# Performance work log

Measured on AMD Instinct MI355X. Metric: run time of the kernel, lower is better.

The kernel has to match this reference:

```python
import jax, jax.numpy as jnp
import numpy as np

B, S, D, H, R = 16, 2048, 1024, 1024, 16


def setup_inputs() -> dict:
    key = jax.random.key(0)
    ks = jax.random.split(key, 6)
    inv = 1.0 / np.sqrt(D)
    return {
        "x": jax.random.normal(ks[0], (B, S, D), jnp.float32),
        "Wa": jax.random.uniform(ks[1], (H, D), jnp.float32, -inv, inv),
        "ba": jnp.zeros((H,), jnp.float32),
        "Wg": jax.random.uniform(ks[2], (R, D), jnp.float32, -inv, inv),
        "bg": jnp.zeros((R,), jnp.float32),
        "Wu": jax.random.uniform(ks[3], (H, D), jnp.float32, -inv, inv),
        "bu": jnp.zeros((H,), jnp.float32),
        "u": jax.random.normal(ks[4], (H, R), jnp.float32) * 0.02,
        "v": jax.random.normal(ks[5], (H, R), jnp.float32) * 0.02,
    }


def reference(x, Wa, ba, Wg, bg, Wu, bu, u, v):
    # Precompute all per-step projections in big GEMMs (same math as the
    # per-step Linear calls in the original loop).
    a = jax.nn.sigmoid(jnp.einsum('bsd,hd->bsh', x, Wa) + ba)   # [B,S,H]
    g = jnp.einsum('bsd,rd->bsr', x, Wg) + bg                    # [B,S,R]
    u_in = jnp.einsum('bsd,hd->bsh', x, Wu) + bu                 # [B,S,H]

    def step(state, ins):
        a_t, g_t, u_t = ins                      # [B,H], [B,R], [B,H]
        low_rank = (state @ v) * g_t             # [B,R]
        state = a_t * state + u_t + low_rank @ u.T
        return state, None

    init = jnp.zeros((x.shape[0], Wa.shape[0]), x.dtype)
    seq = (jnp.swapaxes(a, 0, 1), jnp.swapaxes(g, 0, 1), jnp.swapaxes(u_in, 0, 1))
    state, _ = jax.lax.scan(step, init, seq)
    return state  # [B, H]
```

## Files before the change

### kernel.cpp

```cpp
#include <hip/hip_runtime.h>
#include <hip/hip_bf16.h>
#include <stdint.h>

#define Bb 16
#define Ss 2048
#define Dd 1024
#define Hh 1024
#define Rr 16
#define Mm 32768

typedef __attribute__((ext_vector_type(4))) float f32x4;
typedef __attribute__((ext_vector_type(8))) short bf16x8;

__device__ __forceinline__ unsigned short f2bf(float f) {
    union { float f; uint32_t u; } c; c.f = f;
    uint32_t u = c.u + 0x7fffu + ((c.u >> 16) & 1u);
    return (unsigned short)(u >> 16);
}
__device__ __forceinline__ float bfbits2f(uint32_t bits) {
    union { uint32_t u; float f; } c; c.u = bits << 16; return c.f;
}

__device__ __forceinline__ void gld16(const void* gsrc, void* ldst) {
    __builtin_amdgcn_global_load_lds(
        (const __attribute__((address_space(1))) unsigned int*)gsrc,
        (__attribute__((address_space(3))) unsigned int*)ldst, 16, 0, 0);
}

__device__ __forceinline__ void softbar() {
    __asm volatile("" ::: "memory");
    __builtin_amdgcn_s_waitcnt(0xC07F);
    __builtin_amdgcn_s_barrier();
    __asm volatile("" ::: "memory");
}

__global__ __launch_bounds__(256) void k_convert(
    const float* __restrict__ x, const float* __restrict__ Wa,
    const float* __restrict__ Wu,
    unsigned short* __restrict__ xb, unsigned short* __restrict__ Wab,
    unsigned short* __restrict__ Wub)
{
    long e = ((long)blockIdx.x * 256 + threadIdx.x) * 4;
    const long nx = (long)Mm * Dd;
    const long nw = (long)Hh * Dd;
    const float* src; unsigned short* dst; long o;
    if (e < nx)            { src = x;  dst = xb;  o = e; }
    else if (e < nx + nw)  { src = Wa; dst = Wab; o = e - nx; }
    else                   { src = Wu; dst = Wub; o = e - nx - nw; }
    float4 f = *(const float4*)(src + o);
    ushort4 r;
    r.x = f2bf(f.x); r.y = f2bf(f.y); r.z = f2bf(f.z); r.w = f2bf(f.w);
    *(ushort4*)(dst + o) = r;
}

__global__ __launch_bounds__(256) void k_gemm(
    const unsigned short* __restrict__ Xb,
    const unsigned short* __restrict__ Wab,
    const unsigned short* __restrict__ Wub,
    const float* __restrict__ ba, const float* __restrict__ bu,
    unsigned short* __restrict__ outA, unsigned short* __restrict__ outU)
{
    __shared__ short At[128 * 32];
    __shared__ short Bt[128 * 32];

    const int tid  = threadIdx.x;
    const int lane = tid & 63;
    const int wave = tid >> 6;
    const int bm = blockIdx.x;
    const int bn = blockIdx.y;
    const int region = bn >> 3;
    const int nbase = (bn & 7) * 128;

    const short* Ag = (const short*)Xb;
    const short* Bg = (const short*)(region ? Wub : Wab);
    const float* bias = region ? bu : ba;
    unsigned short* outp = region ? outU : outA;

    const int wm = wave & 1, wn = wave >> 1;
    const int srow = lane >> 2, sseg = lane & 3;
    const int mrow = lane & 15, kb = lane >> 4;

    f32x4 acc[4][4] = {};

    for (int kt = 0; kt < 32; ++kt) {
        __syncthreads();
        const int k0 = kt * 32;
        #pragma unroll
        for (int p = 0; p < 2; ++p) {
            const int row = p * 64 + wave * 16 + srow;
            const short* ga = Ag + (long)(bm * 128 + row) * Dd + k0 + sseg * 8;
            gld16((const void*)ga, (void*)&At[p * 2048 + wave * 512]);
            const short* gb = Bg + (long)(nbase + row) * Dd + k0 + sseg * 8;
            gld16((const void*)gb, (void*)&Bt[p * 2048 + wave * 512]);
        }
        __syncthreads();

        bf16x8 af[4], bq[4];
        #pragma unroll
        for (int i = 0; i < 4; ++i) {
            af[i] = *(const bf16x8*)&At[(wm * 64 + i * 16 + mrow) * 32 + kb * 8];
            bq[i] = *(const bf16x8*)&Bt[(wn * 64 + i * 16 + mrow) * 32 + kb * 8];
        }
        #pragma unroll
        for (int i = 0; i < 4; ++i)
            #pragma unroll
            for (int j = 0; j < 4; ++j)
                acc[i][j] = __builtin_amdgcn_mfma_f32_16x16x32_bf16(
                    af[i], bq[j], acc[i][j], 0, 0, 0);
    }

    const int col = lane & 15, rq = lane >> 4;
    #pragma unroll
    for (int j = 0; j < 4; ++j) {
        const int n = nbase + wn * 64 + j * 16 + col;
        const float bv = bias[n];
        #pragma unroll
        for (int i = 0; i < 4; ++i) {
            const int mb = bm * 128 + wm * 64 + i * 16 + rq * 4;
            #pragma unroll
            for (int r = 0; r < 4; ++r) {
                float vv = acc[i][j][r] + bv;
                if (region == 0) vv = 1.0f / (1.0f + __expf(-vv));
                outp[(long)(mb + r) * Hh + n] = f2bf(vv);
            }
        }
    }
}

__global__ __launch_bounds__(256) void k_g(
    const float* __restrict__ x, const float* __restrict__ Wg,
    const float* __restrict__ bg, float* __restrict__ g)
{
    const int tid = threadIdx.x;
    const int r = tid & 15, ml = tid >> 4;
    const long m = (long)blockIdx.x * 16 + ml;
    const float4* xr = (const float4*)(x + m * Dd);
    const float4* wr = (const float4*)(Wg + (long)r * Dd);
    float acc = 0.0f;
    #pragma unroll 4
    for (int k = 0; k < Dd / 4; ++k) {
        float4 a = xr[k], b = wr[k];
        acc = fmaf(a.x, b.x, acc); acc = fmaf(a.y, b.y, acc);
        acc = fmaf(a.z, b.z, acc); acc = fmaf(a.w, b.w, acc);
    }
    g[m * Rr + r] = acc + bg[r];
}

__global__ __launch_bounds__(1024) void k_scan(
    const unsigned short* __restrict__ a,
    const unsigned short* __restrict__ uin,
    const float* __restrict__ g,
    const float* __restrict__ u,
    const float* __restrict__ v,
    float* __restrict__ out)
{
    __shared__ __align__(16) float sbf[Hh];
    __shared__ __align__(16) float cacc[16 * 20];
    __shared__ __align__(16) float qbuf[16];

    const int tid  = threadIdx.x;
    const int lane = tid & 63;
    const int wave = tid >> 6;
    const int sub  = lane >> 4;
    const int ra   = lane & 15;
    const int b = blockIdx.x;

    const int hA = wave * 64 + sub * 16;
    float vr[16];
    #pragma unroll
    for (int j = 0; j < 16; ++j) vr[j] = v[(hA + j) * Rr + ra];
    float ur[16];
    #pragma unroll
    for (int j = 0; j < 4; ++j) {
        float4 t4 = *(const float4*)&u[tid * Rr + j * 4];
        ur[j*4+0] = t4.x; ur[j*4+1] = t4.y; ur[j*4+2] = t4.z; ur[j*4+3] = t4.w;
    }

    const unsigned short* ap = a   + (long)b * Ss * Hh + tid;
    const unsigned short* up = uin + (long)b * Ss * Hh + tid;
    const float*          gp = g   + (long)b * Ss * Rr + tid;

    float s = 0.0f;
    uint32_t pa[4], pu[4]; float pg[4];
    #pragma unroll
    for (int t = 0; t < 4; ++t) { pa[t] = ap[t * Hh]; pu[t] = up[t * Hh]; }
    ap += 4 * Hh; up += 4 * Hh;
    if (tid < 16) {
        #pragma unroll
        for (int t = 0; t < 4; ++t) pg[t] = gp[t * Rr];
        gp += 4 * Rr;
    }

    sbf[tid] = 0.0f;
    __syncthreads();

    const float* spA = &sbf[hA];

#define STEP(R, PF) do {                                                    \
                                         \
    f32x4 s0 = *(const f32x4*)(spA);                                        \
    f32x4 s1 = *((const f32x4*)(spA) + 1);                                  \
    f32x4 s2 = *((const f32x4*)(spA) + 2);                                  \
    f32x4 s3 = *((const f32x4*)(spA) + 3);                                  \
    float part = s0.x * vr[0];                                              \
    part = fmaf(s0.y, vr[1],  part); part = fmaf(s0.z, vr[2],  part);       \
    part = fmaf(s0.w, vr[3],  part); part = fmaf(s1.x, vr[4],  part);       \
    part = fmaf(s1.y, vr[5],  part); part = fmaf(s1.z, vr[6],  part);       \
    part = fmaf(s1.w, vr[7],  part); part = fmaf(s2.x, vr[8],  part);       \
    part = fmaf(s2.y, vr[9],  part); part = fmaf(s2.z, vr[10], part);       \
    part = fmaf(s2.w, vr[11], part); part = fmaf(s3.x, vr[12], part);       \
    part = fmaf(s3.y, vr[13], part); part = fmaf(s3.z, vr[14], part);       \
    part = fmaf(s3.w, vr[15], part);                                        \
    part += __shfl_xor(part, 16);                                           \
    part += __shfl_xor(part, 32);                                           \
    if (lane < 16) cacc[20 * ra + wave] = part;                             \
    softbar();                                                    \
               \
    if (tid < 16) {                                                         \
        const float* cr = &cacc[20 * tid];                                  \
        f32x4 c0 = *(const f32x4*)(cr);                                     \
        f32x4 c1 = *((const f32x4*)(cr) + 1);                               \
        f32x4 c2 = *((const f32x4*)(cr) + 2);                               \
        f32x4 c3 = *((const f32x4*)(cr) + 3);                               \
        f32x4 cs = (c0 + c1) + (c2 + c3);                                   \
        qbuf[tid] = pg[R] * ((cs.x + cs.y) + (cs.z + cs.w));                \
        if (PF) { pg[R] = *gp; gp += Rr; }                                  \
    }                                                                       \
    softbar();                                                    \
                                   \
    f32x4 q0 = *(const f32x4*)(qbuf);                                       \
    f32x4 q1 = *((const f32x4*)(qbuf) + 1);                                 \
    f32x4 q2 = *((const f32x4*)(qbuf) + 2);                                 \
    f32x4 q3 = *((const f32x4*)(qbuf) + 3);                                 \
    float lr = q0.x * ur[0];                                                \
    lr = fmaf(q0.y, ur[1],  lr); lr = fmaf(q0.z, ur[2],  lr);               \
    lr = fmaf(q0.w, ur[3],  lr); lr = fmaf(q1.x, ur[4],  lr);               \
    lr = fmaf(q1.y, ur[5],  lr); lr = fmaf(q1.z, ur[6],  lr);               \
    lr = fmaf(q1.w, ur[7],  lr); lr = fmaf(q2.x, ur[8],  lr);               \
    lr = fmaf(q2.y, ur[9],  lr); lr = fmaf(q2.z, ur[10], lr);               \
    lr = fmaf(q2.w, ur[11], lr); lr = fmaf(q3.x, ur[12], lr);               \
    lr = fmaf(q3.y, ur[13], lr); lr = fmaf(q3.z, ur[14], lr);               \
    lr = fmaf(q3.w, ur[15], lr);                                            \
    s = fmaf(bfbits2f(pa[R]), s, bfbits2f(pu[R]) + lr);                     \
    sbf[tid] = s;                                                           \
    if (PF) {                                                               \
        pa[R] = *ap; ap += Hh;                                              \
        pu[R] = *up; up += Hh;                                              \
    }                                                                       \
    softbar();                                                    \
} while (0)

    for (int t4 = 0; t4 < Ss / 4 - 1; ++t4) {
        STEP(0, 1); STEP(1, 1); STEP(2, 1); STEP(3, 1);
    }
    STEP(0, 0); STEP(1, 0); STEP(2, 0); STEP(3, 0);
#undef STEP

    out[(long)b * Hh + tid] = s;
}

extern "C" void kernel_launch(void* const* d_in, const int* in_sizes, int n_in,
                              void* d_out, int out_size, void* d_ws, size_t ws_size,
                              hipStream_t stream)
{
    const float* x  = (const float*)d_in[0];
    const float* Wa = (const float*)d_in[1];
    const float* ba = (const float*)d_in[2];
    const float* Wg = (const float*)d_in[3];
    const float* bg = (const float*)d_in[4];
    const float* Wu = (const float*)d_in[5];
    const float* bu = (const float*)d_in[6];
    const float* u  = (const float*)d_in[7];
    const float* v  = (const float*)d_in[8];
    float* out = (float*)d_out;

    char* ws = (char*)d_ws;
    unsigned short* xb   = (unsigned short*)(ws);
    unsigned short* Wab  = (unsigned short*)(ws + 67108864);
    unsigned short* Wub  = (unsigned short*)(ws + 69206016);
    unsigned short* abuf = (unsigned short*)(ws + 71303168);
    unsigned short* ubuf = (unsigned short*)(ws + 138412032);
    float*          gbuf = (float*)(ws + 205520896);

    hipLaunchKernelGGL(k_convert, dim3(34816), dim3(256), 0, stream,
                       x, Wa, Wu, xb, Wab, Wub);
    hipLaunchKernelGGL(k_gemm, dim3(256, 16), dim3(256), 0, stream,
                       xb, Wab, Wub, ba, bu, abuf, ubuf);
    hipLaunchKernelGGL(k_g, dim3(2048), dim3(256), 0, stream,
                       x, Wg, bg, gbuf);
    hipLaunchKernelGGL(k_scan, dim3(Bb), dim3(1024), 0, stream,
                       abuf, ubuf, gbuf, u, v, out);
}
```

Measured before the change: 1.913 ms.

## Halve scan block size, two states per thread, drop one barrier per step

The scan kernel now runs 512 threads, each owning two hidden states, and uses packed float2 math. Every wave computes the 16 low-rank q values redundantly from the cross-wave partial sums and keeps them in a per-wave slot. That replaces the second block-wide barrier with a local LDS wait, cutting per-step synchronisation in the latency-bound serial recurrence. In exchange it does redundant reduction work in every wave and uses more registers per thread.

```diff
diff --git a/kernel.cpp b/kernel.cpp
--- a/kernel.cpp
+++ b/kernel.cpp
@@ -10,6 +10,7 @@
 #define Mm 32768
 
 typedef __attribute__((ext_vector_type(4))) float f32x4;
+typedef __attribute__((ext_vector_type(2))) float f32x2;
 typedef __attribute__((ext_vector_type(8))) short bf16x8;
 
 __device__ __forceinline__ unsigned short f2bf(float f) {
@@ -17,8 +18,11 @@
     uint32_t u = c.u + 0x7fffu + ((c.u >> 16) & 1u);
     return (unsigned short)(u >> 16);
 }
-__device__ __forceinline__ float bfbits2f(uint32_t bits) {
-    union { uint32_t u; float f; } c; c.u = bits << 16; return c.f;
+__device__ __forceinline__ float bflo2f(uint32_t pair) {
+    union { uint32_t u; float f; } c; c.u = pair << 16; return c.f;
+}
+__device__ __forceinline__ float bfhi2f(uint32_t pair) {
+    union { uint32_t u; float f; } c; c.u = pair & 0xffff0000u; return c.f;
 }
 
 __device__ __forceinline__ void gld16(const void* gsrc, void* ldst) {
@@ -31,6 +35,11 @@
     __asm volatile("" ::: "memory");
     __builtin_amdgcn_s_waitcnt(0xC07F);
     __builtin_amdgcn_s_barrier();
+    __asm volatile("" ::: "memory");
+}
+__device__ __forceinline__ void ldsfence() {
+    __asm volatile("" ::: "memory");
+    __builtin_amdgcn_s_waitcnt(0xC07F);
     __asm volatile("" ::: "memory");
 }
 
@@ -146,7 +155,7 @@
     g[m * Rr + r] = acc + bg[r];
 }
 
-__global__ __launch_bounds__(1024) void k_scan(
+__global__ __launch_bounds__(512) void k_scan(
     const unsigned short* __restrict__ a,
     const unsigned short* __restrict__ uin,
     const float* __restrict__ g,
@@ -155,8 +164,8 @@
     float* __restrict__ out)
 {
     __shared__ __align__(16) float sbf[Hh];
-    __shared__ __align__(16) float cacc[16 * 20];
-    __shared__ __align__(16) float qbuf[16];
+    __shared__ __align__(16) float cacc[16 * 12];
+    __shared__ __align__(16) float qw[8 * 20];
 
     const int tid  = threadIdx.x;
     const int lane = tid & 63;
@@ -164,88 +173,84 @@
     const int sub  = lane >> 4;
     const int ra   = lane & 15;
     const int b = blockIdx.x;
-
-    const int hA = wave * 64 + sub * 16;
-    float vr[16];
-    #pragma unroll
-    for (int j = 0; j < 16; ++j) vr[j] = v[(hA + j) * Rr + ra];
-    float ur[16];
-    #pragma unroll
-    for (int j = 0; j < 4; ++j) {
-        float4 t4 = *(const float4*)&u[tid * Rr + j * 4];
-        ur[j*4+0] = t4.x; ur[j*4+1] = t4.y; ur[j*4+2] = t4.z; ur[j*4+3] = t4.w;
-    }
-
-    const unsigned short* ap = a   + (long)b * Ss * Hh + tid;
-    const unsigned short* up = uin + (long)b * Ss * Hh + tid;
-    const float*          gp = g   + (long)b * Ss * Rr + tid;
-
-    float s = 0.0f;
+    const int h0 = 2 * tid;
+
+    const int hA = wave * 128 + sub * 32;
+    f32x2 vr2[16];
+    #pragma unroll
+    for (int k = 0; k < 16; ++k) {
+        f32x2 t;
+        t.x = v[(hA + 2 * k + 0) * Rr + ra];
+        t.y = v[(hA + 2 * k + 1) * Rr + ra];
+        vr2[k] = t;
+    }
+    f32x2 ur2[16];
+    #pragma unroll
+    for (int r = 0; r < 16; ++r) {
+        f32x2 t; t.x = u[h0 * Rr + r]; t.y = u[(h0 + 1) * Rr + r];
+        ur2[r] = t;
+    }
+
+    const uint32_t* ap = (const uint32_t*)(a   + (long)b * Ss * Hh) + tid;
+    const uint32_t* up = (const uint32_t*)(uin + (long)b * Ss * Hh) + tid;
+    const float*    gp = g + (long)b * Ss * Rr + ra;
+
     uint32_t pa[4], pu[4]; float pg[4];
     #pragma unroll
-    for (int t = 0; t < 4; ++t) { pa[t] = ap[t * Hh]; pu[t] = up[t * Hh]; }
-    ap += 4 * Hh; up += 4 * Hh;
-    if (tid < 16) {
-        #pragma unroll
-        for (int t = 0; t < 4; ++t) pg[t] = gp[t * Rr];
-        gp += 4 * Rr;
-    }
-
-    sbf[tid] = 0.0f;
+    for (int t = 0; t < 4; ++t) {
+        pa[t] = ap[t * (Hh / 2)]; pu[t] = up[t * (Hh / 2)]; pg[t] = gp[t * Rr];
+    }
+    ap += 4 * (Hh / 2); up += 4 * (Hh / 2); gp += 4 * Rr;
+
+    f32x2 s2; s2.x = 0.0f; s2.y = 0.0f;
+    *(f32x2*)&sbf[h0] = s2;
     __syncthreads();
 
-    const float* spA = &sbf[hA];
+    const f32x4* spA = (const f32x4*)&sbf[hA];
+    const int caccw = 12 * ra + wave;
+    const f32x4* crow = (const f32x4*)&cacc[12 * ra];
+    float* qslot = &qw[20 * wave + ra];
+    const f32x4* qrow = (const f32x4*)&qw[20 * wave];
 
 #define STEP(R, PF) do {                                                    \
-                                         \
-    f32x4 s0 = *(const f32x4*)(spA);                                        \
-    f32x4 s1 = *((const f32x4*)(spA) + 1);                                  \
-    f32x4 s2 = *((const f32x4*)(spA) + 2);                                  \
-    f32x4 s3 = *((const f32x4*)(spA) + 3);                                  \
-    float part = s0.x * vr[0];                                              \
-    part = fmaf(s0.y, vr[1],  part); part = fmaf(s0.z, vr[2],  part);       \
-    part = fmaf(s0.w, vr[3],  part); part = fmaf(s1.x, vr[4],  part);       \
-    part = fmaf(s1.y, vr[5],  part); part = fmaf(s1.z, vr[6],  part);       \
-    part = fmaf(s1.w, vr[7],  part); part = fmaf(s2.x, vr[8],  part);       \
-    part = fmaf(s2.y, vr[9],  part); part = fmaf(s2.z, vr[10], part);       \
-    part = fmaf(s2.w, vr[11], part); part = fmaf(s3.x, vr[12], part);       \
-    part = fmaf(s3.y, vr[13], part); part = fmaf(s3.z, vr[14], part);       \
-    part = fmaf(s3.w, vr[15], part);                                        \
+                       \
+    f32x4 t0 = spA[0], t1 = spA[1], t2 = spA[2], t3 = spA[3];               \
+    f32x4 t4 = spA[4], t5 = spA[5], t6 = spA[6], t7 = spA[7];               \
+    f32x2 p2 = t0.xy * vr2[0];                                              \
+    p2 += t0.zw * vr2[1];  p2 += t1.xy * vr2[2];  p2 += t1.zw * vr2[3];     \
+    p2 += t2.xy * vr2[4];  p2 += t2.zw * vr2[5];  p2 += t3.xy * vr2[6];     \
+    p2 += t3.zw * vr2[7];  p2 += t4.xy * vr2[8];  p2 += t4.zw * vr2[9];     \
+    p2 += t5.xy * vr2[10]; p2 += t5.zw * vr2[11]; p2 += t6.xy * vr2[12];    \
+    p2 += t6.zw * vr2[13]; p2 += t7.xy * vr2[14]; p2 += t7.zw * vr2[15];    \
+    float part = p2.x + p2.y;                                               \
     part += __shfl_xor(part, 16);                                           \
     part += __shfl_xor(part, 32);                                           \
-    if (lane < 16) cacc[20 * ra + wave] = part;                             \
+    if (lane < 16) cacc[caccw] = part;                                      \
     softbar();                                                    \
-               \
-    if (tid < 16) {                                                         \
-        const float* cr = &cacc[20 * tid];                                  \
-        f32x4 c0 = *(const f32x4*)(cr);                                     \
-        f32x4 c1 = *((const f32x4*)(cr) + 1);                               \
-        f32x4 c2 = *((const f32x4*)(cr) + 2);                               \
-        f32x4 c3 = *((const f32x4*)(cr) + 3);                               \
-        f32x4 cs = (c0 + c1) + (c2 + c3);                                   \
-        qbuf[tid] = pg[R] * ((cs.x + cs.y) + (cs.z + cs.w));                \
-        if (PF) { pg[R] = *gp; gp += Rr; }                                  \
-    }                                                                       \
-    softbar();                                                    \
-                                   \
-    f32x4 q0 = *(const f32x4*)(qbuf);                                       \
-    f32x4 q1 = *((const f32x4*)(qbuf) + 1);                                 \
-    f32x4 q2 = *((const f32x4*)(qbuf) + 2);                                 \
-    f32x4 q3 = *((const f32x4*)(qbuf) + 3);                                 \
-    float lr = q0.x * ur[0];                                                \
-    lr = fmaf(q0.y, ur[1],  lr); lr = fmaf(q0.z, ur[2],  lr);               \
-    lr = fmaf(q0.w, ur[3],  lr); lr = fmaf(q1.x, ur[4],  lr);               \
-    lr = fmaf(q1.y, ur[5],  lr); lr = fmaf(q1.z, ur[6],  lr);               \
-    lr = fmaf(q1.w, ur[7],  lr); lr = fmaf(q2.x, ur[8],  lr);               \
-    lr = fmaf(q2.y, ur[9],  lr); lr = fmaf(q2.z, ur[10], lr);               \
-    lr = fmaf(q2.w, ur[11], lr); lr = fmaf(q3.x, ur[12], lr);               \
-    lr = fmaf(q3.y, ur[13], lr); lr = fmaf(q3.z, ur[14], lr);               \
-    lr = fmaf(q3.w, ur[15], lr);                                            \
-    s = fmaf(bfbits2f(pa[R]), s, bfbits2f(pu[R]) + lr);                     \
-    sbf[tid] = s;                                                           \
+     \
+    f32x4 c0 = crow[0], c1 = crow[1];                                       \
+    f32x4 cs = c0 + c1;                                                     \
+    float q_own = pg[R] * ((cs.x + cs.y) + (cs.z + cs.w));                  \
+    if (sub == 0) *qslot = q_own;                                           \
+    ldsfence();                      \
+    f32x4 q0 = qrow[0], q1 = qrow[1], q2 = qrow[2], q3 = qrow[3];           \
+    f32x2 lr2 = f32x2{q0.x, q0.x} * ur2[0];                                 \
+    lr2 += f32x2{q0.y, q0.y} * ur2[1];  lr2 += f32x2{q0.z, q0.z} * ur2[2];  \
+    lr2 += f32x2{q0.w, q0.w} * ur2[3];  lr2 += f32x2{q1.x, q1.x} * ur2[4];  \
+    lr2 += f32x2{q1.y, q1.y} * ur2[5];  lr2 += f32x2{q1.z, q1.z} * ur2[6];  \
+    lr2 += f32x2{q1.w, q1.w} * ur2[7];  lr2 += f32x2{q2.x, q2.x} * ur2[8];  \
+    lr2 += f32x2{q2.y, q2.y} * ur2[9];  lr2 += f32x2{q2.z, q2.z} * ur2[10]; \
+    lr2 += f32x2{q2.w, q2.w} * ur2[11]; lr2 += f32x2{q3.x, q3.x} * ur2[12]; \
+    lr2 += f32x2{q3.y, q3.y} * ur2[13]; lr2 += f32x2{q3.z, q3.z} * ur2[14]; \
+    lr2 += f32x2{q3.w, q3.w} * ur2[15];                                     \
+    f32x2 av; av.x = bflo2f(pa[R]); av.y = bfhi2f(pa[R]);                   \
+    f32x2 uv; uv.x = bflo2f(pu[R]); uv.y = bfhi2f(pu[R]);                   \
+    s2 = av * s2 + (uv + lr2);                                              \
+    *(f32x2*)&sbf[h0] = s2;                                                 \
     if (PF) {                                                               \
-        pa[R] = *ap; ap += Hh;                                              \
-        pu[R] = *up; up += Hh;                                              \
+        pa[R] = *ap; ap += Hh / 2;                                          \
+        pu[R] = *up; up += Hh / 2;                                          \
+        pg[R] = *gp; gp += Rr;                                              \
     }                                                                       \
     softbar();                                                    \
 } while (0)
@@ -256,7 +261,7 @@
     STEP(0, 0); STEP(1, 0); STEP(2, 0); STEP(3, 0);
 #undef STEP
 
-    out[(long)b * Hh + tid] = s;
+    *(f32x2*)&out[(long)b * Hh + h0] = s2;
 }
 
 extern "C" void kernel_launch(void* const* d_in, const int* in_sizes, int n_in,
@@ -288,6 +293,6 @@
                        xb, Wab, Wub, ba, bu, abuf, ubuf);
     hipLaunchKernelGGL(k_g, dim3(2048), dim3(256), 0, stream,
                        x, Wg, bg, gbuf);
-    hipLaunchKernelGGL(k_scan, dim3(Bb), dim3(1024), 0, stream,
+    hipLaunchKernelGGL(k_scan, dim3(Bb), dim3(512), 0, stream,
                        abuf, ubuf, gbuf, u, v, out);
 }
```

Result: slower. 1.978 ms (+3.4%).
